# Kernel tuning notes

Measured on AMD Instinct MI355X. Metric: run time of the kernel, lower is better.

The kernel has to match this reference:

```python
import jax, jax.numpy as jnp
import numpy as np

P = 16          # patch size
NUM_HEADS = 8
WINDOW = 64     # window_size from SparseAttention(window_size=64)


def _layer_norm(x, w, b, eps=1e-5):
    mu = jnp.mean(x, axis=-1, keepdims=True)
    var = jnp.var(x, axis=-1, keepdims=True)
    return (x - mu) * jax.lax.rsqrt(var + eps) * w + b


def _sinusoidal_pe(num_patches, num_features, dtype):
    pos = jnp.arange(num_patches, dtype=jnp.float32)[:, None]            # [N,1]
    i = jnp.arange(0, num_features, 2, dtype=jnp.float32)                # [D/2]
    div = jnp.exp(-jnp.log(10000.0) * i / num_features)                  # [D/2]
    ang = pos * div                                                      # [N,D/2]
    pe = jnp.stack([jnp.sin(ang), jnp.cos(ang)], axis=-1).reshape(num_patches, num_features)
    return pe.astype(dtype)


def _ffn(x, w1, b1, w2, b2):
    # FeedForward: Linear -> GELU -> Linear (dropout inactive at eval)
    h = jax.nn.gelu(jnp.einsum('bnd,hd->bnh', x, w1) + b1)
    return jnp.einsum('bnh,dh->bnd', h, w2) + b2


def _windowed_attention(x, qkv_w, qkv_b, proj_w, proj_b):
    B, N, D = x.shape
    hd = D // NUM_HEADS
    qkv = jnp.einsum('bnd,ed->bne', x, qkv_w) + qkv_b                    # [B,N,3D]
    qkv = qkv.reshape(B, N, 3, NUM_HEADS, hd)
    q, k, v = qkv[:, :, 0], qkv[:, :, 1], qkv[:, :, 2]                   # [B,N,H,hd]
    nw = N // WINDOW
    # partition sequence into non-overlapping windows of 64 tokens
    q = q.reshape(B, nw, WINDOW, NUM_HEADS, hd).transpose(0, 3, 1, 2, 4)  # [B,H,nw,W,hd]
    k = k.reshape(B, nw, WINDOW, NUM_HEADS, hd).transpose(0, 3, 1, 2, 4)
    v = v.reshape(B, nw, WINDOW, NUM_HEADS, hd).transpose(0, 3, 1, 2, 4)
    scale = 1.0 / jnp.sqrt(jnp.asarray(hd, x.dtype))
    scores = jnp.einsum('bhwqd,bhwkd->bhwqk', q, k) * scale              # [B,H,nw,W,W]
    attn = jax.nn.softmax(scores, axis=-1)
    out = jnp.einsum('bhwqk,bhwkd->bhwqd', attn, v)                      # [B,H,nw,W,hd]
    out = out.transpose(0, 2, 3, 1, 4).reshape(B, N, D)
    return jnp.einsum('bnd,ed->bne', out, proj_w) + proj_b


def setup_inputs() -> dict:
    key = jax.random.key(0)
    ks = jax.random.split(key, 8)
    D, HF = 256, 1024
    s = lambda fan: 1.0 / np.sqrt(fan)
    return {
        'x': jax.random.normal(ks[0], (32, 3, 512, 512), jnp.float32),
        'conv_w': jax.random.normal(ks[1], (D, 3, P, P), jnp.float32) * s(3 * P * P),
        'conv_b': jnp.zeros((D,), jnp.float32),
        'ln_w': jnp.ones((D,), jnp.float32),
        'ln_b': jnp.zeros((D,), jnp.float32),
        'qkv_w': jax.random.normal(ks[2], (3 * D, D), jnp.float32) * s(D),
        'qkv_b': jnp.zeros((3 * D,), jnp.float32),
        'proj_w': jax.random.normal(ks[3], (D, D), jnp.float32) * s(D),
        'proj_b': jnp.zeros((D,), jnp.float32),
        'ff_w1': jax.random.normal(ks[4], (HF, D), jnp.float32) * s(D),
        'ff_b1': jnp.zeros((HF,), jnp.float32),
        'ff_w2': jax.random.normal(ks[5], (D, HF), jnp.float32) * s(HF),
        'ff_b2': jnp.zeros((D,), jnp.float32),
    }


def reference(x, conv_w, conv_b, ln_w, ln_b, qkv_w, qkv_b, proj_w, proj_b,
              ff_w1, ff_b1, ff_w2, ff_b2):
    B, C, H, W = x.shape
    D = conv_w.shape[0]
    # PatchEmbedding1: Conv2d(C, D, kernel=16, stride=16) == per-patch matmul, then LayerNorm
    nH, nW = H // P, W // P
    patches = x.reshape(B, C, nH, P, nW, P).transpose(0, 2, 4, 1, 3, 5).reshape(B, nH * nW, C * P * P)
    h = jnp.einsum('bnp,dp->bnd', patches, conv_w.reshape(D, -1)) + conv_b
    h = _layer_norm(h, ln_w, ln_b)
    # static sinusoidal position embedding
    h = h + _sinusoidal_pe(h.shape[1], D, h.dtype)
    # block 1: FFN -> sparse (windowed) attention -> residual
    identity = h
    h = _ffn(h, ff_w1, ff_b1, ff_w2, ff_b2)
    h = _windowed_attention(h, qkv_w, qkv_b, proj_w, proj_b)
    h = h + identity
    # block 2: shared FFN -> residual
    identity = h
    h = _ffn(h, ff_w1, ff_b1, ff_w2, ff_b2)
    return h + identity
```

## Files before the change

### kernel.cpp

```cpp
#include <hip/hip_runtime.h>
#include <math.h>


#define M_TOK 32768

typedef __attribute__((ext_vector_type(8))) short  short8;
typedef __attribute__((ext_vector_type(4))) float  f32x4;
typedef __attribute__((ext_vector_type(8))) unsigned short us8v;
typedef __attribute__((ext_vector_type(4))) unsigned short us4v;

__device__ __forceinline__ unsigned short f2b(float f) {
    union { float f; unsigned u; } c; c.f = f;
    unsigned r = c.u + 0x7fffu + ((c.u >> 16) & 1u);
    return (unsigned short)(r >> 16);
}
__device__ __forceinline__ float b2f(unsigned short u) {
    union { unsigned u; float f; } c; c.u = ((unsigned)u) << 16;
    return c.f;
}
__device__ __forceinline__ float gelu_fast(float x) {
    const float c0 = 0.7978845608028654f;
    const float c1 = 0.044715f * 0.7978845608028654f;
    float z = x * (c0 + c1 * x * x);
    float e = __expf(-2.0f * z);
    return x * __builtin_amdgcn_rcpf(1.0f + e);
}
__device__ __forceinline__ void load_lds16(const unsigned short* g, void* lds) {
    __builtin_amdgcn_global_load_lds(
        (const __attribute__((address_space(1))) unsigned int*)g,
        (__attribute__((address_space(3))) unsigned int*)lds, 16, 0, 0);
}

__global__ __launch_bounds__(256) void cvt_f2b_kernel(
    const float* __restrict__ in, unsigned short* __restrict__ out, int n)
{
    int i = (blockIdx.x * 256 + threadIdx.x) * 4;
    if (i >= n) return;
    float4 v = *(const float4*)(in + i);
    us4v o;
    o[0] = f2b(v.x); o[1] = f2b(v.y); o[2] = f2b(v.z); o[3] = f2b(v.w);
    *(us4v*)(out + i) = o;
}

__global__ __launch_bounds__(256) void pe_init_kernel(float* __restrict__ pe)
{
    const int pos = blockIdx.x;
    const int d   = threadIdx.x;
    const int ieven = d & ~1;
    float div = expf(-9.210340371976184f * (float)ieven * (1.0f / 256.0f));
    float ang = (float)pos * div;
    pe[pos * 256 + d] = (d & 1) ? cosf(ang) : sinf(ang);
}

template<bool GELU, bool RES, bool WF32, bool WB16>
__global__ __launch_bounds__(256) void mfma_gemm_kernel(
    const unsigned short* __restrict__ A, const unsigned short* __restrict__ W,
    const float* __restrict__ bias, const unsigned short* __restrict__ res,
    float* __restrict__ outF, unsigned short* __restrict__ outB,
    int M, int N, int K)
{
    __shared__ unsigned short As[128 * 32];
    __shared__ unsigned short Ws[128 * 32];

    const int t    = threadIdx.x;
    const int m0   = blockIdx.y * 128;
    const int n0   = blockIdx.x * 128;
    const int wv   = t >> 6, lane = t & 63;
    const int wr   = (wv >> 1) * 64, wc = (wv & 1) * 64;
    const int l15  = lane & 15, quad = lane >> 4;

    f32x4 acc[4][4];
#pragma unroll
    for (int i = 0; i < 4; i++)
#pragma unroll
        for (int j = 0; j < 4; j++)
#pragma unroll
            for (int r = 0; r < 4; r++) acc[i][j][r] = 0.0f;

    const int srow = wv * 16 + (lane >> 2);
    const int skk  = (lane & 3) * 8;
    const unsigned short* gA0 = A + (size_t)(m0 + srow) * K + skk;
    const unsigned short* gA1 = gA0 + (size_t)64 * K;
    const unsigned short* gW0 = W + (size_t)(n0 + srow) * K + skk;
    const unsigned short* gW1 = gW0 + (size_t)64 * K;
    char* lA0 = (char*)As + wv * 1024;
    char* lA1 = lA0 + 4096;
    char* lW0 = (char*)Ws + wv * 1024;
    char* lW1 = lW0 + 4096;

    for (int k0 = 0; k0 < K; k0 += 32) {
        __syncthreads();
        load_lds16(gA0 + k0, lA0);
        load_lds16(gA1 + k0, lA1);
        load_lds16(gW0 + k0, lW0);
        load_lds16(gW1 + k0, lW1);
        __syncthreads();

        short8 af[4], wf[4];
#pragma unroll
        for (int i = 0; i < 4; i++)
            af[i] = *(const short8*)&As[(wr + i * 16 + l15) * 32 + quad * 8];
#pragma unroll
        for (int j = 0; j < 4; j++)
            wf[j] = *(const short8*)&Ws[(wc + j * 16 + l15) * 32 + quad * 8];
#pragma unroll
        for (int i = 0; i < 4; i++)
#pragma unroll
            for (int j = 0; j < 4; j++)
                acc[i][j] = __builtin_amdgcn_mfma_f32_16x16x32_bf16(
                    wf[j], af[i], acc[i][j], 0, 0, 0);
    }

#pragma unroll
    for (int i = 0; i < 4; i++) {
        const int gr = m0 + wr + i * 16 + l15;
#pragma unroll
        for (int j = 0; j < 4; j++) {
            const int gc = n0 + wc + j * 16 + quad * 4;
            const float4 bv = *(const float4*)&bias[gc];
            float v0 = acc[i][j][0] + bv.x;
            float v1 = acc[i][j][1] + bv.y;
            float v2 = acc[i][j][2] + bv.z;
            float v3 = acc[i][j][3] + bv.w;
            if (GELU) {
                v0 = gelu_fast(v0); v1 = gelu_fast(v1);
                v2 = gelu_fast(v2); v3 = gelu_fast(v3);
            }
            if (RES) {
                us4v rv = *(const us4v*)&res[(size_t)gr * N + gc];
                v0 += b2f(rv[0]); v1 += b2f(rv[1]);
                v2 += b2f(rv[2]); v3 += b2f(rv[3]);
            }
            if (WF32) {
                float4 o; o.x = v0; o.y = v1; o.z = v2; o.w = v3;
                *(float4*)&outF[(size_t)gr * N + gc] = o;
            }
            if (WB16) {
                us4v o;
                o[0] = f2b(v0); o[1] = f2b(v1); o[2] = f2b(v2); o[3] = f2b(v3);
                *(us4v*)&outB[(size_t)gr * N + gc] = o;
            }
        }
    }
}

__global__ __launch_bounds__(256) void patch_mfma_kernel(
    const unsigned short* __restrict__ xb, const unsigned short* __restrict__ W,
    const float* __restrict__ bias, unsigned short* __restrict__ outB)
{
    __shared__ unsigned short As[128 * 32];
    __shared__ unsigned short Ws[128 * 32];

    const int t    = threadIdx.x;
    const int m0   = blockIdx.y * 128;
    const int n0   = blockIdx.x * 128;
    const int wv   = t >> 6, lane = t & 63;
    const int wr   = (wv >> 1) * 64, wc = (wv & 1) * 64;
    const int l15  = lane & 15, quad = lane >> 4;

    f32x4 acc[4][4];
#pragma unroll
    for (int i = 0; i < 4; i++)
#pragma unroll
        for (int j = 0; j < 4; j++)
#pragma unroll
            for (int r = 0; r < 4; r++) acc[i][j][r] = 0.0f;

    const int srow = wv * 16 + (lane >> 2);
    const int skk  = (lane & 3) * 8;
    size_t xoff[2];
#pragma unroll
    for (int s = 0; s < 2; s++) {
        const int m  = m0 + s * 64 + srow;
        const int b  = m >> 10;
        const int idx = m & 1023;
        const int hh = idx >> 5, ww = idx & 31;
        xoff[s] = ((size_t)(b * 3) * 512 + (size_t)(hh * 16)) * 512 + ww * 16;
    }
    const unsigned short* gW0 = W + (size_t)(n0 + srow) * 768 + skk;
    const unsigned short* gW1 = gW0 + (size_t)64 * 768;
    char* lA0 = (char*)As + wv * 1024;
    char* lA1 = lA0 + 4096;
    char* lW0 = (char*)Ws + wv * 1024;
    char* lW1 = lW0 + 4096;

    for (int k0 = 0; k0 < 768; k0 += 32) {
        const int k  = k0 + skk;
        const int c  = k >> 8;
        const int ph = (k >> 4) & 15;
        const int pw = k & 15;
        const size_t koff = (size_t)c * 262144 + (size_t)ph * 512 + pw;
        __syncthreads();
        load_lds16(xb + xoff[0] + koff, lA0);
        load_lds16(xb + xoff[1] + koff, lA1);
        load_lds16(gW0 + k0, lW0);
        load_lds16(gW1 + k0, lW1);
        __syncthreads();

        short8 af[4], wf[4];
#pragma unroll
        for (int i = 0; i < 4; i++)
            af[i] = *(const short8*)&As[(wr + i * 16 + l15) * 32 + quad * 8];
#pragma unroll
        for (int j = 0; j < 4; j++)
            wf[j] = *(const short8*)&Ws[(wc + j * 16 + l15) * 32 + quad * 8];
#pragma unroll
        for (int i = 0; i < 4; i++)
#pragma unroll
            for (int j = 0; j < 4; j++)
                acc[i][j] = __builtin_amdgcn_mfma_f32_16x16x32_bf16(
                    wf[j], af[i], acc[i][j], 0, 0, 0);
    }

#pragma unroll
    for (int i = 0; i < 4; i++) {
        const int gr = m0 + wr + i * 16 + l15;
#pragma unroll
        for (int j = 0; j < 4; j++) {
            const int gc = n0 + wc + j * 16 + quad * 4;
            const float4 bv = *(const float4*)&bias[gc];
            us4v o;
            o[0] = f2b(acc[i][j][0] + bv.x);
            o[1] = f2b(acc[i][j][1] + bv.y);
            o[2] = f2b(acc[i][j][2] + bv.z);
            o[3] = f2b(acc[i][j][3] + bv.w);
            *(us4v*)&outB[(size_t)gr * 256 + gc] = o;
        }
    }
}

__global__ __launch_bounds__(256) void ln_pe_kernel(
    const unsigned short* __restrict__ in, const float* __restrict__ w,
    const float* __restrict__ b, const float* __restrict__ pe_t,
    unsigned short* __restrict__ outB)
{
    const int m = blockIdx.x;
    const int d = threadIdx.x;
    float v = b2f(in[(size_t)m * 256 + d]);

    float s = v, s2 = v * v;
#pragma unroll
    for (int off = 32; off > 0; off >>= 1) {
        s  += __shfl_down(s,  off, 64);
        s2 += __shfl_down(s2, off, 64);
    }
    __shared__ float ss[4], ss2[4], stats[2];
    const int lane = d & 63, wid = d >> 6;
    if (lane == 0) { ss[wid] = s; ss2[wid] = s2; }
    __syncthreads();
    if (d == 0) {
        float a  = ss[0] + ss[1] + ss[2] + ss[3];
        float a2 = ss2[0] + ss2[1] + ss2[2] + ss2[3];
        float mean = a * (1.0f / 256.0f);
        float var  = a2 * (1.0f / 256.0f) - mean * mean;
        stats[0] = mean;
        stats[1] = rsqrtf(var + 1e-5f);
    }
    __syncthreads();
    const float mean = stats[0], rstd = stats[1];

    const int pos = m & 1023;
    float pe = pe_t[pos * 256 + d];

    float o = (v - mean) * rstd * w[d] + b[d] + pe;
    outB[(size_t)m * 256 + d] = f2b(o);
}

__global__ __launch_bounds__(256) void attn_mfma_kernel(
    const unsigned short* __restrict__ qkv, unsigned short* __restrict__ out)
{
    __shared__ unsigned short Ps[64 * 72];
    __shared__ unsigned short Vt[32 * 72];

    const int blk = blockIdx.x;
    const int h = blk & 7;
    const int w = (blk >> 3) & 15;
    const int b = blk >> 7;
    const int m_base = b * 1024 + w * 64;

    const int t = threadIdx.x;
    const int wv = t >> 6, lane = t & 63;
    const int l15 = lane & 15, quad = lane >> 4;

    {
        const int row = t >> 2;
        const int c0  = (t & 3) * 8;
        const unsigned short* src = qkv + (size_t)(m_base + row) * 768 + 512 + h * 32 + c0;
        us8v v = *(const us8v*)src;
#pragma unroll
        for (int j = 0; j < 8; j++) Vt[(c0 + j) * 72 + row] = v[j];
    }

    short8 aq = *(const short8*)(qkv + (size_t)(m_base + wv * 16 + l15) * 768 + h * 32 + quad * 8);
    f32x4 c[4];
#pragma unroll
    for (int j = 0; j < 4; j++) {
        short8 bk = *(const short8*)(qkv + (size_t)(m_base + j * 16 + l15) * 768 + 256 + h * 32 + quad * 8);
        f32x4 z = {0.0f, 0.0f, 0.0f, 0.0f};
        c[j] = __builtin_amdgcn_mfma_f32_16x16x32_bf16(aq, bk, z, 0, 0, 0);
    }

    const float scale = 0.17677669529663687f;
    float sm[4];
#pragma unroll
    for (int r = 0; r < 4; r++) {
        float m0 = -1e30f;
#pragma unroll
        for (int j = 0; j < 4; j++) { c[j][r] *= scale; m0 = fmaxf(m0, c[j][r]); }
#pragma unroll
        for (int d = 1; d < 16; d <<= 1) m0 = fmaxf(m0, __shfl_xor(m0, d, 64));
        float s0 = 0.0f;
#pragma unroll
        for (int j = 0; j < 4; j++) { float e = __expf(c[j][r] - m0); c[j][r] = e; s0 += e; }
#pragma unroll
        for (int d = 1; d < 16; d <<= 1) s0 += __shfl_xor(s0, d, 64);
        sm[r] = __builtin_amdgcn_rcpf(s0);
    }

#pragma unroll
    for (int r = 0; r < 4; r++) {
        const int prow = wv * 16 + quad * 4 + r;
#pragma unroll
        for (int j = 0; j < 4; j++)
            Ps[prow * 72 + j * 16 + l15] = f2b(c[j][r] * sm[r]);
    }
    __syncthreads();

    short8 ap0 = *(const short8*)&Ps[(wv * 16 + l15) * 72 + quad * 8];
    short8 ap1 = *(const short8*)&Ps[(wv * 16 + l15) * 72 + 32 + quad * 8];
    f32x4 o[2];
#pragma unroll
    for (int nt = 0; nt < 2; nt++) {
        short8 bv0 = *(const short8*)&Vt[(nt * 16 + l15) * 72 + quad * 8];
        short8 bv1 = *(const short8*)&Vt[(nt * 16 + l15) * 72 + 32 + quad * 8];
        f32x4 z = {0.0f, 0.0f, 0.0f, 0.0f};
        o[nt] = __builtin_amdgcn_mfma_f32_16x16x32_bf16(ap0, bv0, z, 0, 0, 0);
        o[nt] = __builtin_amdgcn_mfma_f32_16x16x32_bf16(ap1, bv1, o[nt], 0, 0, 0);
    }

#pragma unroll
    for (int nt = 0; nt < 2; nt++) {
#pragma unroll
        for (int r = 0; r < 4; r++) {
            const int row = m_base + wv * 16 + quad * 4 + r;
            out[(size_t)row * 256 + h * 32 + nt * 16 + l15] = f2b(o[nt][r]);
        }
    }
}

extern "C" void kernel_launch(void* const* d_in, const int* in_sizes, int n_in,
                              void* d_out, int out_size, void* d_ws, size_t ws_size,
                              hipStream_t stream)
{
    const float* x      = (const float*)d_in[0];
    const float* conv_w = (const float*)d_in[1];
    const float* conv_b = (const float*)d_in[2];
    const float* ln_w   = (const float*)d_in[3];
    const float* ln_b   = (const float*)d_in[4];
    const float* qkv_w  = (const float*)d_in[5];
    const float* qkv_b  = (const float*)d_in[6];
    const float* proj_w = (const float*)d_in[7];
    const float* proj_b = (const float*)d_in[8];
    const float* ff_w1  = (const float*)d_in[9];
    const float* ff_b1  = (const float*)d_in[10];
    const float* ff_w2  = (const float*)d_in[11];
    const float* ff_b2  = (const float*)d_in[12];
    float* out = (float*)d_out;

    char* ws = (char*)d_ws;
    unsigned short* xb    = (unsigned short*)(ws);
    unsigned short* hidb  = (unsigned short*)(ws);
    unsigned short* h0b   = (unsigned short*)(ws + 67108864);
    unsigned short* qkvb  = (unsigned short*)(ws + 67108864);
    float*          pe_t  = (float*)(ws + 117440512);
    unsigned short* h1b   = (unsigned short*)(ws + 118489088);
    unsigned short* f1b   = (unsigned short*)(ws + 135266304);
    unsigned short* h2b   = (unsigned short*)(ws + 152043520);
    unsigned short* aob   = (unsigned short*)(ws + 168820736);
    unsigned short* wbase = (unsigned short*)(ws + 185597952);
    unsigned short* conv_wb = wbase;
    unsigned short* qkv_wb  = wbase + 196608;
    unsigned short* proj_wb = wbase + 393216;
    unsigned short* ff_w1b  = wbase + 458752;
    unsigned short* ff_w2b  = wbase + 720896;

    const int M = M_TOK;
    dim3 blk(256);

    cvt_f2b_kernel<<<dim3(25165824 / 1024), blk, 0, stream>>>(x, xb, 25165824);
    cvt_f2b_kernel<<<dim3(196608 / 1024), blk, 0, stream>>>(conv_w, conv_wb, 196608);
    cvt_f2b_kernel<<<dim3(196608 / 1024), blk, 0, stream>>>(qkv_w, qkv_wb, 196608);
    cvt_f2b_kernel<<<dim3(65536 / 1024), blk, 0, stream>>>(proj_w, proj_wb, 65536);
    cvt_f2b_kernel<<<dim3(262144 / 1024), blk, 0, stream>>>(ff_w1, ff_w1b, 262144);
    cvt_f2b_kernel<<<dim3(262144 / 1024), blk, 0, stream>>>(ff_w2, ff_w2b, 262144);
    pe_init_kernel<<<dim3(1024), blk, 0, stream>>>(pe_t);

    patch_mfma_kernel<<<dim3(2, M / 128), blk, 0, stream>>>(xb, conv_wb, conv_b, h0b);
    ln_pe_kernel<<<dim3(M), blk, 0, stream>>>(h0b, ln_w, ln_b, pe_t, h1b);
    mfma_gemm_kernel<true, false, false, true><<<dim3(8, M / 128), blk, 0, stream>>>(
        h1b, ff_w1b, ff_b1, nullptr, nullptr, hidb, M, 1024, 256);
    mfma_gemm_kernel<false, false, false, true><<<dim3(2, M / 128), blk, 0, stream>>>(
        hidb, ff_w2b, ff_b2, nullptr, nullptr, f1b, M, 256, 1024);
    mfma_gemm_kernel<false, false, false, true><<<dim3(6, M / 128), blk, 0, stream>>>(
        f1b, qkv_wb, qkv_b, nullptr, nullptr, qkvb, M, 768, 256);
    attn_mfma_kernel<<<dim3(4096), blk, 0, stream>>>(qkvb, aob);
    mfma_gemm_kernel<false, true, false, true><<<dim3(2, M / 128), blk, 0, stream>>>(
        aob, proj_wb, proj_b, h1b, nullptr, h2b, M, 256, 256);
    mfma_gemm_kernel<true, false, false, true><<<dim3(8, M / 128), blk, 0, stream>>>(
        h2b, ff_w1b, ff_b1, nullptr, nullptr, hidb, M, 1024, 256);
    mfma_gemm_kernel<false, true, true, false><<<dim3(2, M / 128), blk, 0, stream>>>(
        hidb, ff_w2b, ff_b2, h2b, out, nullptr, M, 256, 1024);
}
```

Baseline: 467.1 us.

## Fuse FFN up/down GEMMs into one kernel keeping hidden activations on-chip

Adds an ffn_fused_kernel that keeps a 128-token input tile in LDS and walks the 1024-wide hidden dimension in chunks of 32. Each chunk is computed with MFMA, passed through bias+GELU, staged per-wave in LDS, and immediately accumulated into the 256-wide output. This removes the 32768x1024 bf16 hidden-tensor write and re-read for both FFN passes. It also merges the five weight-conversion launches into one and compacts the workspace layout. In exchange, it uses large LDS and register footprints (16x2 output accumulators per wave), which may limit occupancy. W1 and W2 are read straight from global memory without LDS reuse.

```diff
diff --git a/kernel.cpp b/kernel.cpp
--- a/kernel.cpp
+++ b/kernel.cpp
@@ -42,6 +42,24 @@
     *(us4v*)(out + i) = o;
 }
 
+__global__ __launch_bounds__(256) void cvt_weights_kernel(
+    const float* __restrict__ s0, const float* __restrict__ s1,
+    const float* __restrict__ s2, const float* __restrict__ s3,
+    const float* __restrict__ s4, unsigned short* __restrict__ dst)
+{
+    int i = (blockIdx.x * 256 + threadIdx.x) * 4;
+    const float* src; int off;
+    if      (i < 196608) { src = s0; off = 0; }
+    else if (i < 393216) { src = s1; off = 196608; }
+    else if (i < 458752) { src = s2; off = 393216; }
+    else if (i < 720896) { src = s3; off = 458752; }
+    else                 { src = s4; off = 720896; }
+    float4 v = *(const float4*)(src + (i - off));
+    us4v o;
+    o[0] = f2b(v.x); o[1] = f2b(v.y); o[2] = f2b(v.z); o[3] = f2b(v.w);
+    *(us4v*)(dst + i) = o;
+}
+
 __global__ __launch_bounds__(256) void pe_init_kernel(float* __restrict__ pe)
 {
     const int pos = blockIdx.x;
@@ -52,12 +70,124 @@
     pe[pos * 256 + d] = (d & 1) ? cosf(ang) : sinf(ang);
 }
 
-template<bool GELU, bool RES, bool WF32, bool WB16>
+#define ALD 272
+template<bool RES>
+__global__ __launch_bounds__(256, 2) void ffn_fused_kernel(
+    const unsigned short* __restrict__ A, const unsigned short* __restrict__ W1,
+    const float* __restrict__ b1, const unsigned short* __restrict__ W2,
+    const float* __restrict__ b2, const unsigned short* __restrict__ res,
+    float* __restrict__ outF, unsigned short* __restrict__ outB)
+{
+    __shared__ unsigned short As[128 * ALD];
+    __shared__ unsigned short Hs[4][32 * 40];
+
+    const int t    = threadIdx.x;
+    const int wv   = t >> 6, lane = t & 63;
+    const int l15  = lane & 15, quad = lane >> 4;
+    const int m0   = blockIdx.x * 128;
+
+    {
+        const int col = (t & 31) * 8;
+        const int r0  = t >> 5;
+#pragma unroll
+        for (int it = 0; it < 16; it++) {
+            const int row = it * 8 + r0;
+            us8v v = *(const us8v*)(A + (size_t)(m0 + row) * 256 + col);
+            *(us8v*)&As[row * ALD + col] = v;
+        }
+    }
+    __syncthreads();
+
+    f32x4 oacc[2][16];
+#pragma unroll
+    for (int i = 0; i < 2; i++)
+#pragma unroll
+        for (int n = 0; n < 16; n++)
+#pragma unroll
+            for (int r = 0; r < 4; r++) oacc[i][n][r] = 0.0f;
+
+    const int arow0 = (wv * 32      + l15) * ALD + quad * 8;
+    const int arow1 = (wv * 32 + 16 + l15) * ALD + quad * 8;
+    unsigned short* hsw = &Hs[wv][0];
+
+    for (int c = 0; c < 32; c++) {
+        f32x4 acc1[2][2];
+#pragma unroll
+        for (int i = 0; i < 2; i++)
+#pragma unroll
+            for (int f = 0; f < 2; f++)
+#pragma unroll
+                for (int r = 0; r < 4; r++) acc1[i][f][r] = 0.0f;
+
+        const unsigned short* w1p = W1 + (size_t)(c * 32 + l15) * 256 + quad * 8;
+#pragma unroll
+        for (int kk = 0; kk < 8; kk++) {
+            short8 a0  = *(const short8*)&As[arow0 + kk * 32];
+            short8 a1  = *(const short8*)&As[arow1 + kk * 32];
+            short8 w0  = *(const short8*)(w1p + kk * 32);
+            short8 w1v = *(const short8*)(w1p + 16 * 256 + kk * 32);
+            acc1[0][0] = __builtin_amdgcn_mfma_f32_16x16x32_bf16(w0,  a0, acc1[0][0], 0, 0, 0);
+            acc1[0][1] = __builtin_amdgcn_mfma_f32_16x16x32_bf16(w1v, a0, acc1[0][1], 0, 0, 0);
+            acc1[1][0] = __builtin_amdgcn_mfma_f32_16x16x32_bf16(w0,  a1, acc1[1][0], 0, 0, 0);
+            acc1[1][1] = __builtin_amdgcn_mfma_f32_16x16x32_bf16(w1v, a1, acc1[1][1], 0, 0, 0);
+        }
+
+#pragma unroll
+        for (int i = 0; i < 2; i++)
+#pragma unroll
+            for (int f = 0; f < 2; f++) {
+                const float4 bb = *(const float4*)&b1[c * 32 + f * 16 + quad * 4];
+                us4v hv;
+                hv[0] = f2b(gelu_fast(acc1[i][f][0] + bb.x));
+                hv[1] = f2b(gelu_fast(acc1[i][f][1] + bb.y));
+                hv[2] = f2b(gelu_fast(acc1[i][f][2] + bb.z));
+                hv[3] = f2b(gelu_fast(acc1[i][f][3] + bb.w));
+                *(us4v*)&hsw[(i * 16 + l15) * 40 + f * 16 + quad * 4] = hv;
+            }
+
+        short8 h0 = *(const short8*)&hsw[ l15       * 40 + quad * 8];
+        short8 h1 = *(const short8*)&hsw[(16 + l15) * 40 + quad * 8];
+
+        const unsigned short* w2p = W2 + (size_t)l15 * 1024 + c * 32 + quad * 8;
+#pragma unroll
+        for (int n = 0; n < 16; n++) {
+            short8 wf = *(const short8*)(w2p + (size_t)n * 16384);
+            oacc[0][n] = __builtin_amdgcn_mfma_f32_16x16x32_bf16(wf, h0, oacc[0][n], 0, 0, 0);
+            oacc[1][n] = __builtin_amdgcn_mfma_f32_16x16x32_bf16(wf, h1, oacc[1][n], 0, 0, 0);
+        }
+    }
+
+#pragma unroll
+    for (int i = 0; i < 2; i++) {
+        const int gr = m0 + wv * 32 + i * 16 + l15;
+#pragma unroll
+        for (int n = 0; n < 16; n++) {
+            const int gc = n * 16 + quad * 4;
+            const float4 bb = *(const float4*)&b2[gc];
+            float v0 = oacc[i][n][0] + bb.x;
+            float v1 = oacc[i][n][1] + bb.y;
+            float v2 = oacc[i][n][2] + bb.z;
+            float v3 = oacc[i][n][3] + bb.w;
+            if (RES) {
+                us4v rv = *(const us4v*)&res[(size_t)gr * 256 + gc];
+                v0 += b2f(rv[0]); v1 += b2f(rv[1]);
+                v2 += b2f(rv[2]); v3 += b2f(rv[3]);
+                float4 o; o.x = v0; o.y = v1; o.z = v2; o.w = v3;
+                *(float4*)&outF[(size_t)gr * 256 + gc] = o;
+            } else {
+                us4v o;
+                o[0] = f2b(v0); o[1] = f2b(v1); o[2] = f2b(v2); o[3] = f2b(v3);
+                *(us4v*)&outB[(size_t)gr * 256 + gc] = o;
+            }
+        }
+    }
+}
+
+template<bool RES>
 __global__ __launch_bounds__(256) void mfma_gemm_kernel(
     const unsigned short* __restrict__ A, const unsigned short* __restrict__ W,
     const float* __restrict__ bias, const unsigned short* __restrict__ res,
-    float* __restrict__ outF, unsigned short* __restrict__ outB,
-    int M, int N, int K)
+    unsigned short* __restrict__ outB, int M, int N, int K)
 {
     __shared__ unsigned short As[128 * 32];
     __shared__ unsigned short Ws[128 * 32];
@@ -122,24 +252,14 @@
             float v1 = acc[i][j][1] + bv.y;
             float v2 = acc[i][j][2] + bv.z;
             float v3 = acc[i][j][3] + bv.w;
-            if (GELU) {
-                v0 = gelu_fast(v0); v1 = gelu_fast(v1);
-                v2 = gelu_fast(v2); v3 = gelu_fast(v3);
-            }
             if (RES) {
                 us4v rv = *(const us4v*)&res[(size_t)gr * N + gc];
                 v0 += b2f(rv[0]); v1 += b2f(rv[1]);
                 v2 += b2f(rv[2]); v3 += b2f(rv[3]);
             }
-            if (WF32) {
-                float4 o; o.x = v0; o.y = v1; o.z = v2; o.w = v3;
-                *(float4*)&outF[(size_t)gr * N + gc] = o;
-            }
-            if (WB16) {
-                us4v o;
-                o[0] = f2b(v0); o[1] = f2b(v1); o[2] = f2b(v2); o[3] = f2b(v3);
-                *(us4v*)&outB[(size_t)gr * N + gc] = o;
-            }
+            us4v o;
+            o[0] = f2b(v0); o[1] = f2b(v1); o[2] = f2b(v2); o[3] = f2b(v3);
+            *(us4v*)&outB[(size_t)gr * N + gc] = o;
         }
     }
 }
@@ -369,15 +489,14 @@
 
     char* ws = (char*)d_ws;
     unsigned short* xb    = (unsigned short*)(ws);
-    unsigned short* hidb  = (unsigned short*)(ws);
-    unsigned short* h0b   = (unsigned short*)(ws + 67108864);
-    unsigned short* qkvb  = (unsigned short*)(ws + 67108864);
-    float*          pe_t  = (float*)(ws + 117440512);
-    unsigned short* h1b   = (unsigned short*)(ws + 118489088);
-    unsigned short* f1b   = (unsigned short*)(ws + 135266304);
-    unsigned short* h2b   = (unsigned short*)(ws + 152043520);
-    unsigned short* aob   = (unsigned short*)(ws + 168820736);
-    unsigned short* wbase = (unsigned short*)(ws + 185597952);
+    unsigned short* qkvb  = (unsigned short*)(ws);
+    unsigned short* h0b   = (unsigned short*)(ws + 50331648);
+    unsigned short* f1b   = (unsigned short*)(ws + 50331648);
+    unsigned short* h1b   = (unsigned short*)(ws + 67108864);
+    unsigned short* h2b   = (unsigned short*)(ws + 67108864);
+    unsigned short* aob   = (unsigned short*)(ws + 83886080);
+    float*          pe_t  = (float*)(ws + 100663296);
+    unsigned short* wbase = (unsigned short*)(ws + 101711872);
     unsigned short* conv_wb = wbase;
     unsigned short* qkv_wb  = wbase + 196608;
     unsigned short* proj_wb = wbase + 393216;
@@ -388,26 +507,19 @@
     dim3 blk(256);
 
     cvt_f2b_kernel<<<dim3(25165824 / 1024), blk, 0, stream>>>(x, xb, 25165824);
-    cvt_f2b_kernel<<<dim3(196608 / 1024), blk, 0, stream>>>(conv_w, conv_wb, 196608);
-    cvt_f2b_kernel<<<dim3(196608 / 1024), blk, 0, stream>>>(qkv_w, qkv_wb, 196608);
-    cvt_f2b_kernel<<<dim3(65536 / 1024), blk, 0, stream>>>(proj_w, proj_wb, 65536);
-    cvt_f2b_kernel<<<dim3(262144 / 1024), blk, 0, stream>>>(ff_w1, ff_w1b, 262144);
-    cvt_f2b_kernel<<<dim3(262144 / 1024), blk, 0, stream>>>(ff_w2, ff_w2b, 262144);
+    cvt_weights_kernel<<<dim3(983040 / 1024), blk, 0, stream>>>(
+        conv_w, qkv_w, proj_w, ff_w1, ff_w2, wbase);
     pe_init_kernel<<<dim3(1024), blk, 0, stream>>>(pe_t);
 
     patch_mfma_kernel<<<dim3(2, M / 128), blk, 0, stream>>>(xb, conv_wb, conv_b, h0b);
     ln_pe_kernel<<<dim3(M), blk, 0, stream>>>(h0b, ln_w, ln_b, pe_t, h1b);
-    mfma_gemm_kernel<true, false, false, true><<<dim3(8, M / 128), blk, 0, stream>>>(
-        h1b, ff_w1b, ff_b1, nullptr, nullptr, hidb, M, 1024, 256);
-    mfma_gemm_kernel<false, false, false, true><<<dim3(2, M / 128), blk, 0, stream>>>(
-        hidb, ff_w2b, ff_b2, nullptr, nullptr, f1b, M, 256, 1024);
-    mfma_gemm_kernel<false, false, false, true><<<dim3(6, M / 128), blk, 0, stream>>>(
-        f1b, qkv_wb, qkv_b, nullptr, nullptr, qkvb, M, 768, 256);
+    ffn_fused_kernel<false><<<dim3(M / 128), blk, 0, stream>>>(
+        h1b, ff_w1b, ff_b1, ff_w2b, ff_b2, nullptr, nullptr, f1b);
+    mfma_gemm_kernel<false><<<dim3(6, M / 128), blk, 0, stream>>>(
+        f1b, qkv_wb, qkv_b, nullptr, qkvb, M, 768, 256);
     attn_mfma_kernel<<<dim3(4096), blk, 0, stream>>>(qkvb, aob);
-    mfma_gemm_kernel<false, true, false, true><<<dim3(2, M / 128), blk, 0, stream>>>(
-        aob, proj_wb, proj_b, h1b, nullptr, h2b, M, 256, 256);
-    mfma_gemm_kernel<true, false, false, true><<<dim3(8, M / 128), blk, 0, stream>>>(
-        h2b, ff_w1b, ff_b1, nullptr, nullptr, hidb, M, 1024, 256);
-    mfma_gemm_kernel<false, true, true, false><<<dim3(2, M / 128), blk, 0, stream>>>(
-        hidb, ff_w2b, ff_b2, h2b, out, nullptr, M, 256, 1024);
-}
+    mfma_gemm_kernel<true><<<dim3(2, M / 128), blk, 0, stream>>>(
+        aob, proj_wb, proj_b, h1b, h2b, M, 256, 256);
+    ffn_fused_kernel<true><<<dim3(M / 128), blk, 0, stream>>>(
+        h2b, ff_w1b, ff_b1, ff_w2b, ff_b2, h2b, out, nullptr);
+}
```

New measurement: 602.6 us. +29.0%, slower.
